# Kernel optimization log

Measured on AMD Instinct MI355X. Metric: run time of the kernel, lower is better.

The kernel has to match this reference:

```python
import jax, jax.numpy as jnp
import numpy as np

DMODEL = 1024
Q_HEADS = 16
KV_HEADS = 4
DHEAD = 64
SEQ = 2048
TOP_K = 64
ROPE_BASE = 10000.0
NEG_INF = -1e30  # stand-in for -inf that is safe under softmax


def rope_cos_sin(seq_len, dhead, base):
    inv_freq = 1.0 / (base ** (jnp.arange(0, dhead, 2, dtype=jnp.float32) / dhead))  # [dhead/2]
    t = jnp.arange(seq_len, dtype=jnp.float32)
    angles = jnp.outer(t, inv_freq)                       # [S, dhead/2]
    emb = jnp.concatenate([angles, angles], axis=-1)      # [S, dhead]
    return jnp.cos(emb), jnp.sin(emb)


def rotate_half(x):
    x1, x2 = jnp.split(x, 2, axis=-1)
    return jnp.concatenate([-x2, x1], axis=-1)


def apply_rope(x, cos, sin):
    # x: [B, H, S, dhead]; cos/sin: [S, dhead]
    return x * cos[None, None] + rotate_half(x) * sin[None, None]


def setup_inputs() -> dict:
    key = jax.random.key(0)
    ks = jax.random.split(key, 5)
    s = 0.02
    return {
        "x": jax.random.normal(ks[0], (1, SEQ, DMODEL), jnp.float32),
        "Wq": jax.random.normal(ks[1], (Q_HEADS * DHEAD, DMODEL), jnp.float32) * s,
        "Wk": jax.random.normal(ks[2], (KV_HEADS * DHEAD, DMODEL), jnp.float32) * s,
        "Wv": jax.random.normal(ks[3], (KV_HEADS * DHEAD, DMODEL), jnp.float32) * s,
        "Wo": jax.random.normal(ks[4], (DMODEL, Q_HEADS * DHEAD), jnp.float32) * s,
    }


def reference(x, Wq, Wk, Wv, Wo):
    B, S, _ = x.shape
    cos, sin = rope_cos_sin(S, DHEAD, ROPE_BASE)

    q = (x @ Wq.T).reshape(B, S, Q_HEADS, DHEAD).transpose(0, 2, 1, 3)   # [B,Hq,S,d]
    k = (x @ Wk.T).reshape(B, S, KV_HEADS, DHEAD).transpose(0, 2, 1, 3)  # [B,Hkv,S,d]
    v = (x @ Wv.T).reshape(B, S, KV_HEADS, DHEAD).transpose(0, 2, 1, 3)

    q = apply_rope(q, cos, sin)
    k = apply_rope(k, cos, sin)

    groups = Q_HEADS // KV_HEADS  # repeat_kv
    k = jnp.repeat(k, groups, axis=1)  # [B,Hq,S,d]
    v = jnp.repeat(v, groups, axis=1)

    scores = jnp.einsum("bhqd,bhkd->bhqk", q, k) / np.sqrt(DHEAD)  # [B,H,S,S]

    causal_mask = jnp.triu(jnp.ones((S, S), bool), k=1)
    scores = jnp.where(causal_mask[None, None], NEG_INF, scores)

    # top-k mask before softmax
    topk_vals, _ = jax.lax.top_k(scores, TOP_K)            # [B,H,S,K]
    threshold = topk_vals[..., -1:]                         # kth largest
    scores = jnp.where(scores < threshold, NEG_INF, scores)

    weights = jax.nn.softmax(scores, axis=-1)
    out = jnp.einsum("bhqk,bhkd->bhqd", weights, v)         # [B,H,S,d]
    out = out.transpose(0, 2, 1, 3).reshape(B, S, Q_HEADS * DHEAD)
    return out @ Wo.T
```

## Files before the change

### kernel.cpp

```cpp
#include <hip/hip_runtime.h>
#include <hip/hip_bf16.h>
#include <math.h>

#define SEQ 2048
#define DMODEL 1024
#define QH 16
#define KVH 4
#define DH 64
#define TOPK 64
#define KV_D (KVH * DH)
#define CAP 128
#define SROW 1028

typedef __attribute__((ext_vector_type(8))) short short8;
typedef __attribute__((ext_vector_type(4))) float floatx4;

__device__ __forceinline__ unsigned f2u(float f) {
    unsigned u = __float_as_uint(f);
    return (u & 0x80000000u) ? ~u : (u | 0x80000000u);
}
__device__ __forceinline__ float u2f(unsigned u) {
    unsigned v = (u & 0x80000000u) ? (u & 0x7fffffffu) : ~u;
    return __uint_as_float(v);
}
__device__ __forceinline__ unsigned short f2bf(float x) {
    unsigned u = __float_as_uint(x);
    return (unsigned short)((u + 0x7fffu + ((u >> 16) & 1u)) >> 16);
}
__device__ __forceinline__ float bf2f(unsigned short h) {
    return __uint_as_float((unsigned)h << 16);
}
__device__ __forceinline__ void split4(float4 f, ushort4& h, ushort4& l) {
    h.x = f2bf(f.x); l.x = f2bf(f.x - bf2f(h.x));
    h.y = f2bf(f.y); l.y = f2bf(f.y - bf2f(h.y));
    h.z = f2bf(f.z); l.z = f2bf(f.z - bf2f(h.z));
    h.w = f2bf(f.w); l.w = f2bf(f.w - bf2f(h.w));
}

__global__ __launch_bounds__(256) void cvt_all(const float* __restrict__ x,
                                               const float* __restrict__ Wq,
                                               const float* __restrict__ Wk,
                                               const float* __restrict__ Wv,
                                               const float* __restrict__ Wo,
                                               unsigned short* __restrict__ xhi,
                                               unsigned short* __restrict__ xlo,
                                               unsigned short* __restrict__ wbhi,
                                               unsigned short* __restrict__ wblo,
                                               unsigned short* __restrict__ wo) {
    int idx = blockIdx.x * 256 + threadIdx.x;
    if (idx >= 1179648) return;
    float4 f;
    ushort4 h, l;
    if (idx < 524288) {
        f = ((const float4*)x)[idx];
        split4(f, h, l);
        ((ushort4*)xhi)[idx] = h;
        ((ushort4*)xlo)[idx] = l;
    } else if (idx < 786432) {
        int s = idx - 524288;
        f = ((const float4*)Wq)[s];
        split4(f, h, l);
        ((ushort4*)wbhi)[s] = h;
        ((ushort4*)wblo)[s] = l;
    } else if (idx < 851968) {
        int s = idx - 786432;
        f = ((const float4*)Wk)[s];
        split4(f, h, l);
        ((ushort4*)wbhi)[idx - 524288] = h;
        ((ushort4*)wblo)[idx - 524288] = l;
    } else if (idx < 917504) {
        int s = idx - 851968;
        f = ((const float4*)Wv)[s];
        split4(f, h, l);
        ((ushort4*)wbhi)[idx - 524288] = h;
        ((ushort4*)wblo)[idx - 524288] = l;
    } else {
        int s = idx - 917504;
        f = ((const float4*)Wo)[s];
        ushort4 o;
        o.x = f2bf(f.x); o.y = f2bf(f.y); o.z = f2bf(f.z); o.w = f2bf(f.w);
        ((ushort4*)wo)[s] = o;
    }
}

__global__ __launch_bounds__(256) void sincos_lut(float* __restrict__ cosT,
                                                  float* __restrict__ sinT) {
    int idx = blockIdx.x * 256 + threadIdx.x;
    if (idx >= SEQ * 32) return;
    int t = idx >> 5, d = idx & 31;
    float inv = powf(10000.0f, -(float)d * (1.0f / 32.0f));
    float s, c;
    sincosf((float)t * inv, &s, &c);
    cosT[idx] = c;
    sinT[idx] = s;
}

__device__ __forceinline__ void async16(const void* g, void* l) {
    __builtin_amdgcn_global_load_lds(
        (const __attribute__((address_space(1))) unsigned int*)g,
        (__attribute__((address_space(3))) unsigned int*)l, 16, 0, 0);
}

__global__ __launch_bounds__(256, 2) void gemm_qkv(const unsigned short* __restrict__ Ah,
                                                   const unsigned short* __restrict__ Al,
                                                   const unsigned short* __restrict__ Bh,
                                                   const unsigned short* __restrict__ Bl,
                                                   const float* __restrict__ cosT,
                                                   const float* __restrict__ sinT,
                                                   unsigned short* __restrict__ qhi,
                                                   unsigned short* __restrict__ qlo,
                                                   unsigned short* __restrict__ khi,
                                                   unsigned short* __restrict__ klo,
                                                   float* __restrict__ vv) {
    const int K = DMODEL;
    __shared__ unsigned short lAh[128 * 32];
    __shared__ unsigned short lAl[128 * 32];
    __shared__ unsigned short lBh[128 * 32];
    __shared__ unsigned short lBl[128 * 32];
    const int tid = threadIdx.x;
    const int lane = tid & 63;
    const int wid = tid >> 6;
    const int m0 = blockIdx.y * 128, n0 = blockIdx.x * 128;
    const int mq = (wid >> 1) * 64, nq = (wid & 1) * 64;

    floatx4 acc[4][4];
#pragma unroll
    for (int a = 0; a < 4; ++a)
#pragma unroll
        for (int b = 0; b < 4; ++b) acc[a][b] = (floatx4){0.f, 0.f, 0.f, 0.f};

    const int srow = tid >> 2;
    const int skb = (tid & 3) ^ ((tid >> 3) & 3);
    const size_t goff = (size_t)srow * K + skb * 8;
    const size_t goff2 = goff + (size_t)64 * K;
    const unsigned short* pAh = Ah + (size_t)m0 * K;
    const unsigned short* pAl = Al + (size_t)m0 * K;
    const unsigned short* pBh = Bh + (size_t)n0 * K;
    const unsigned short* pBl = Bl + (size_t)n0 * K;
    unsigned lbase = __builtin_amdgcn_readfirstlane((unsigned)(wid * 1024));

    for (int k0 = 0; k0 < K; k0 += 32) {
        async16(pAh + goff + k0, (char*)lAh + lbase);
        async16(pAh + goff2 + k0, (char*)lAh + lbase + 4096);
        async16(pAl + goff + k0, (char*)lAl + lbase);
        async16(pAl + goff2 + k0, (char*)lAl + lbase + 4096);
        async16(pBh + goff + k0, (char*)lBh + lbase);
        async16(pBh + goff2 + k0, (char*)lBh + lbase + 4096);
        async16(pBl + goff + k0, (char*)lBl + lbase);
        async16(pBl + goff2 + k0, (char*)lBl + lbase + 4096);
        __syncthreads();

        short8 ah[4], al[4], bh[4], bl[4];
#pragma unroll
        for (int mt = 0; mt < 4; ++mt) {
            int row = mq + mt * 16 + (lane & 15);
            int s = ((lane >> 4) ^ ((row >> 1) & 3)) * 8;
            ah[mt] = *(const short8*)&lAh[row * 32 + s];
            al[mt] = *(const short8*)&lAl[row * 32 + s];
        }
#pragma unroll
        for (int nt = 0; nt < 4; ++nt) {
            int row = nq + nt * 16 + (lane & 15);
            int s = ((lane >> 4) ^ ((row >> 1) & 3)) * 8;
            bh[nt] = *(const short8*)&lBh[row * 32 + s];
            bl[nt] = *(const short8*)&lBl[row * 32 + s];
        }
#pragma unroll
        for (int mt = 0; mt < 4; ++mt)
#pragma unroll
            for (int nt = 0; nt < 4; ++nt) {
                floatx4 a = acc[mt][nt];
                a = __builtin_amdgcn_mfma_f32_16x16x32_bf16(al[mt], bh[nt], a, 0, 0, 0);
                a = __builtin_amdgcn_mfma_f32_16x16x32_bf16(ah[mt], bl[nt], a, 0, 0, 0);
                a = __builtin_amdgcn_mfma_f32_16x16x32_bf16(ah[mt], bh[nt], a, 0, 0, 0);
                acc[mt][nt] = a;
            }
        __syncthreads();
    }

    if (n0 < 1280) {
        const bool isq = (n0 < 1024);
#pragma unroll
        for (int mt = 0; mt < 4; ++mt)
#pragma unroll
            for (int nt = 0; nt < 2; ++nt) {
                const int d32 = nt * 16 + (lane & 15);
#pragma unroll
                for (int rr = 0; rr < 4; ++rr) {
                    int row = m0 + mq + mt * 16 + (lane >> 4) * 4 + rr;
                    float lo = acc[mt][nt][rr], hi = acc[mt][nt + 2][rr];
                    float c = cosT[row * 32 + d32], s = sinT[row * 32 + d32];
                    float rlo = lo * c - hi * s;
                    float rhi = hi * c + lo * s;
                    unsigned short hlo = f2bf(rlo), hhi = f2bf(rhi);
                    unsigned short llo = f2bf(rlo - bf2f(hlo));
                    unsigned short lhi = f2bf(rhi - bf2f(hhi));
                    if (isq) {
                        size_t o = (size_t)row * DMODEL + n0 + nq + d32;
                        qhi[o] = hlo; qhi[o + 32] = hhi;
                        qlo[o] = llo; qlo[o + 32] = lhi;
                    } else {
                        int kvh = (n0 + nq - 1024) >> 6;
                        size_t o = ((size_t)kvh * SEQ + row) * DH + d32;
                        khi[o] = hlo; khi[o + 32] = hhi;
                        klo[o] = llo; klo[o + 32] = lhi;
                    }
                }
            }
    } else {
#pragma unroll
        for (int mt = 0; mt < 4; ++mt)
#pragma unroll
            for (int nt = 0; nt < 4; ++nt) {
                int vcol = n0 + nq + nt * 16 + (lane & 15) - 1280;
                int rbase = m0 + mq + mt * 16 + (lane >> 4) * 4;
#pragma unroll
                for (int rr = 0; rr < 4; ++rr)
                    vv[(size_t)(rbase + rr) * KV_D + vcol] = acc[mt][nt][rr];
            }
    }
}

__global__ __launch_bounds__(256, 2) void gemm_mfma(const unsigned short* __restrict__ A,
                                                    const unsigned short* __restrict__ B,
                                                    float* __restrict__ C,
                                                    int M, int N, int K) {
    __shared__ unsigned short ldsA[128 * 32];
    __shared__ unsigned short ldsB[128 * 32];
    const int tid = threadIdx.x;
    const int lane = tid & 63;
    const int wid = tid >> 6;
    const int m0 = blockIdx.y * 128, n0 = blockIdx.x * 128;
    const int mq = (wid >> 1) * 64, nq = (wid & 1) * 64;

    floatx4 acc[4][4];
#pragma unroll
    for (int a = 0; a < 4; ++a)
#pragma unroll
        for (int b = 0; b < 4; ++b) acc[a][b] = (floatx4){0.f, 0.f, 0.f, 0.f};

    const int srow = tid >> 2;
    const int skb = (tid & 3) ^ ((tid >> 3) & 3);
    const unsigned short* Ag = A + (size_t)(m0 + srow) * K + skb * 8;
    const unsigned short* Bg = B + (size_t)(n0 + srow) * K + skb * 8;
    unsigned lbase = __builtin_amdgcn_readfirstlane((unsigned)(wid * 1024));
    char* la = (char*)ldsA + lbase;
    char* lb = (char*)ldsB + lbase;

    for (int k0 = 0; k0 < K; k0 += 32) {
        async16(Ag + k0, la);
        async16(Ag + (size_t)64 * K + k0, la + 4096);
        async16(Bg + k0, lb);
        async16(Bg + (size_t)64 * K + k0, lb + 4096);
        __syncthreads();

        short8 af[4], bf[4];
#pragma unroll
        for (int mt = 0; mt < 4; ++mt) {
            int row = mq + mt * 16 + (lane & 15);
            int s = ((lane >> 4) ^ ((row >> 1) & 3)) * 8;
            af[mt] = *(const short8*)&ldsA[row * 32 + s];
        }
#pragma unroll
        for (int nt = 0; nt < 4; ++nt) {
            int row = nq + nt * 16 + (lane & 15);
            int s = ((lane >> 4) ^ ((row >> 1) & 3)) * 8;
            bf[nt] = *(const short8*)&ldsB[row * 32 + s];
        }
#pragma unroll
        for (int mt = 0; mt < 4; ++mt)
#pragma unroll
            for (int nt = 0; nt < 4; ++nt)
                acc[mt][nt] = __builtin_amdgcn_mfma_f32_16x16x32_bf16(af[mt], bf[nt], acc[mt][nt], 0, 0, 0);
        __syncthreads();
    }
#pragma unroll
    for (int mt = 0; mt < 4; ++mt)
#pragma unroll
        for (int nt = 0; nt < 4; ++nt) {
            int col = n0 + nq + nt * 16 + (lane & 15);
            int rbase = m0 + mq + mt * 16 + (lane >> 4) * 4;
#pragma unroll
            for (int rr = 0; rr < 4; ++rr)
                C[(size_t)(rbase + rr) * N + col] = acc[mt][nt][rr];
        }
}

__device__ __forceinline__ void av_group(float w, int jbase, const float* __restrict__ vb,
                                         float& acc) {
    unsigned long long mk = __ballot(w > 0.f);
    while (mk) {
        int l = __ffsll((unsigned long long)mk) - 1;
        mk &= mk - 1;
        float wj = __shfl(w, l, 64);
        acc += wj * vb[(size_t)(jbase + l * 4) * KV_D];
    }
}

__device__ __forceinline__ void score_chunk(const unsigned short* __restrict__ khi,
                                            const unsigned short* __restrict__ klo,
                                            float* __restrict__ S,
                                            const short8& ah0, const short8& ah1,
                                            const short8& al0, const short8& al1,
                                            int kvh, int w, int lane, int imax, int cbase) {
    const int koff = (lane >> 4) * 8;
#pragma unroll
    for (int n = 0; n < 4; ++n) {
        int jbi = cbase + w + n * 16;
        int jb = jbi * 16;
        if (jb <= imax) {
            size_t bidx = ((size_t)kvh * SEQ + jb + (lane & 15)) * DH + koff;
            short8 bh0 = *(const short8*)(khi + bidx);
            short8 bh1 = *(const short8*)(khi + bidx + 32);
            short8 bl0 = *(const short8*)(klo + bidx);
            short8 bl1 = *(const short8*)(klo + bidx + 32);
            floatx4 acc = (floatx4){0.f, 0.f, 0.f, 0.f};
            acc = __builtin_amdgcn_mfma_f32_16x16x32_bf16(al0, bh0, acc, 0, 0, 0);
            acc = __builtin_amdgcn_mfma_f32_16x16x32_bf16(al1, bh1, acc, 0, 0, 0);
            acc = __builtin_amdgcn_mfma_f32_16x16x32_bf16(ah0, bl0, acc, 0, 0, 0);
            acc = __builtin_amdgcn_mfma_f32_16x16x32_bf16(ah1, bl1, acc, 0, 0, 0);
            acc = __builtin_amdgcn_mfma_f32_16x16x32_bf16(ah0, bh0, acc, 0, 0, 0);
            acc = __builtin_amdgcn_mfma_f32_16x16x32_bf16(ah1, bh1, acc, 0, 0, 0);
            int col = (jb & 1023) + (lane & 15);
            int rbase = (lane >> 4) * 4;
#pragma unroll
            for (int rr = 0; rr < 4; ++rr)
                S[(size_t)(rbase + rr) * SROW + col] = acc[rr] * 0.125f;
        }
    }
}

__global__ __launch_bounds__(1024, 8) void attn_block(const unsigned short* __restrict__ qhi,
                                                      const unsigned short* __restrict__ qlo,
                                                      const unsigned short* __restrict__ khi,
                                                      const unsigned short* __restrict__ klo,
                                                      const float* __restrict__ v,
                                                      unsigned short* __restrict__ outb) {
    extern __shared__ float S[];
    const int lane = threadIdx.x & 63;
    const int w = threadIdx.x >> 6;
    const int t = 127 - blockIdx.x;
    const int h = blockIdx.y;
    const int kvh = h >> 2;
    const int m0 = t * 16;
    const int imax = m0 + 15;

    const int arow = m0 + (lane & 15);
    const int koff = (lane >> 4) * 8;
    size_t aidx = (size_t)arow * DMODEL + h * DH + koff;
    short8 ah0 = *(const short8*)(qhi + aidx);
    short8 ah1 = *(const short8*)(qhi + aidx + 32);
    short8 al0 = *(const short8*)(qlo + aidx);
    short8 al1 = *(const short8*)(qlo + aidx + 32);

    const int irow = m0 + w;
    const int cmax = (irow >> 8) + 1;
    float* Srow = S + (size_t)w * SROW;
    uint4 uv[8];
#pragma unroll
    for (int c = 0; c < 8; ++c) uv[c] = make_uint4(0u, 0u, 0u, 0u);

    score_chunk(khi, klo, S, ah0, ah1, al0, al1, kvh, w, lane, imax, 0);
    __syncthreads();
#pragma unroll
    for (int c = 0; c < 4; ++c) {
        if (c < cmax) {
            const int j0 = c * 256 + lane * 4;
            float4 f = *(const float4*)&Srow[j0];
            uv[c].x = (j0 + 0 <= irow) ? f2u(f.x) : 0u;
            uv[c].y = (j0 + 1 <= irow) ? f2u(f.y) : 0u;
            uv[c].z = (j0 + 2 <= irow) ? f2u(f.z) : 0u;
            uv[c].w = (j0 + 3 <= irow) ? f2u(f.w) : 0u;
        }
    }
    __syncthreads();

    if (imax >= 1024) {
        score_chunk(khi, klo, S, ah0, ah1, al0, al1, kvh, w, lane, imax, 64);
    }
    __syncthreads();
#pragma unroll
    for (int c = 4; c < 8; ++c) {
        if (c < cmax) {
            const int j0 = (c - 4) * 256 + lane * 4;
            float4 f = *(const float4*)&Srow[j0];
            int jg = c * 256 + lane * 4;
            uv[c].x = (jg + 0 <= irow) ? f2u(f.x) : 0u;
            uv[c].y = (jg + 1 <= irow) ? f2u(f.y) : 0u;
            uv[c].z = (jg + 2 <= irow) ? f2u(f.z) : 0u;
            uv[c].w = (jg + 3 <= irow) ? f2u(f.w) : 0u;
        }
    }
    __syncthreads();

    float2* pl = (float2*)S + w * CAP;

    unsigned lmax = 0u;
#pragma unroll
    for (int c = 0; c < 8; ++c)
        lmax = max(lmax, max(max(uv[c].x, uv[c].y), max(uv[c].z, uv[c].w)));
    unsigned um = lmax, Lb = lmax;
#pragma unroll
    for (int o = 32; o > 0; o >>= 1) {
        um = max(um, (unsigned)__shfl_xor((int)um, o, 64));
        Lb = min(Lb, (unsigned)__shfl_xor((int)Lb, o, 64));
    }
    const float mf = u2f(um);

    unsigned p = 1u;
    if (irow >= TOPK) {
        unsigned diff = Lb ^ um;
        if (diff == 0u) {
            p = um;
        } else {
            int hb = 31 - __builtin_clz(diff);
            p = (hb >= 31) ? 0u : ((um >> (hb + 1)) << (hb + 1));
            for (int b = hb; b >= 0; --b) {
                unsigned cand = p | (1u << b);
                int cnt = 0;
#pragma unroll
                for (int c = 0; c < 8; ++c) {
                    if (c < cmax) {
                        cnt += __popcll(__ballot(uv[c].x >= cand));
                        cnt += __popcll(__ballot(uv[c].y >= cand));
                        cnt += __popcll(__ballot(uv[c].z >= cand));
                        cnt += __popcll(__ballot(uv[c].w >= cand));
                    }
                }
                if (cnt >= TOPK) p = cand;
            }
        }
    }

    const unsigned long long lmask = (lane == 0) ? 0ull : (~0ull >> (64 - lane));
    int base = 0;
#pragma unroll
    for (int c = 0; c < 8; ++c) {
        if (c < cmax) {
#pragma unroll
            for (int e = 0; e < 4; ++e) {
                unsigned u = (e == 0) ? uv[c].x : (e == 1) ? uv[c].y : (e == 2) ? uv[c].z : uv[c].w;
                bool keep = (u >= p);
                unsigned long long mk = __ballot(keep);
                if (keep) {
                    int pos = base + __popcll(mk & lmask);
                    if (pos < CAP)
                        pl[pos] = make_float2(__expf(u2f(u) - mf),
                                              __int_as_float(c * 256 + lane * 4 + e));
                }
                base += (int)__popcll(mk);
            }
        }
    }

    const float* vb = v + kvh * DH + lane;
    float acc = 0.f, den = 0.f;
    if (base <= CAP) {
        int l = 0;
        for (; l + 16 <= base; l += 16) {
            float2 pr[16];
            float vx[16];
#pragma unroll
            for (int u = 0; u < 16; ++u) pr[u] = pl[l + u];
#pragma unroll
            for (int u = 0; u < 16; ++u)
                vx[u] = vb[(size_t)__float_as_int(pr[u].y) * KV_D];
#pragma unroll
            for (int u = 0; u < 16; ++u) { den += pr[u].x; acc += pr[u].x * vx[u]; }
        }
        for (; l < base; ++l) {
            float2 pp = pl[l];
            den += pp.x;
            acc += pp.x * vb[(size_t)__float_as_int(pp.y) * KV_D];
        }
    } else {
        float lsum = 0.f;
#pragma unroll
        for (int c = 0; c < 8; ++c) {
            if (c < cmax) {
                float w0 = (uv[c].x >= p) ? __expf(u2f(uv[c].x) - mf) : 0.f;
                float w1 = (uv[c].y >= p) ? __expf(u2f(uv[c].y) - mf) : 0.f;
                float w2 = (uv[c].z >= p) ? __expf(u2f(uv[c].z) - mf) : 0.f;
                float w3 = (uv[c].w >= p) ? __expf(u2f(uv[c].w) - mf) : 0.f;
                lsum += (w0 + w1) + (w2 + w3);
                av_group(w0, c * 256 + 0, vb, acc);
                av_group(w1, c * 256 + 1, vb, acc);
                av_group(w2, c * 256 + 2, vb, acc);
                av_group(w3, c * 256 + 3, vb, acc);
            }
        }
        den = lsum;
#pragma unroll
        for (int o = 32; o > 0; o >>= 1) den += __shfl_xor(den, o, 64);
    }

    outb[(size_t)irow * DMODEL + h * DH + lane] = f2bf(acc / den);
}

extern "C" void kernel_launch(void* const* d_in, const int* in_sizes, int n_in,
                              void* d_out, int out_size, void* d_ws, size_t ws_size,
                              hipStream_t stream) {
    const float* x  = (const float*)d_in[0];
    const float* Wq = (const float*)d_in[1];
    const float* Wk = (const float*)d_in[2];
    const float* Wv = (const float*)d_in[3];
    const float* Wo = (const float*)d_in[4];
    float* out = (float*)d_out;

    float* ws = (float*)d_ws;
    float* vv   = ws;
    float* cosT = vv + (size_t)SEQ * KV_D;
    float* sinT = cosT + SEQ * 32;
    unsigned short* bfp = (unsigned short*)(sinT + SEQ * 32);
    unsigned short* xhi  = bfp;  bfp += (size_t)SEQ * DMODEL;
    unsigned short* xlo  = bfp;  bfp += (size_t)SEQ * DMODEL;
    unsigned short* wbhi = bfp;  bfp += (size_t)1536 * DMODEL;
    unsigned short* wblo = bfp;  bfp += (size_t)1536 * DMODEL;
    unsigned short* wob  = bfp;  bfp += (size_t)DMODEL * DMODEL;
    unsigned short* qhi  = bfp;  bfp += (size_t)SEQ * DMODEL;
    unsigned short* qlo  = bfp;  bfp += (size_t)SEQ * DMODEL;
    unsigned short* khi  = bfp;  bfp += (size_t)KVH * SEQ * DH;
    unsigned short* klo  = bfp;  bfp += (size_t)KVH * SEQ * DH;
    unsigned short* attnb = xhi;

    dim3 blk(256);

    cvt_all<<<(1179648 + 255) / 256, blk, 0, stream>>>(x, Wq, Wk, Wv, Wo,
                                                       xhi, xlo, wbhi, wblo, wob);
    sincos_lut<<<(SEQ * 32 + 255) / 256, blk, 0, stream>>>(cosT, sinT);

    gemm_qkv<<<dim3(1536 / 128, SEQ / 128), blk, 0, stream>>>(xhi, xlo, wbhi, wblo,
                                                              cosT, sinT,
                                                              qhi, qlo, khi, klo, vv);

    const int attn_lds = 16 * SROW * 4;
    hipFuncSetAttribute((const void*)attn_block,
                        hipFuncAttributeMaxDynamicSharedMemorySize, attn_lds);
    attn_block<<<dim3(SEQ / 16, QH), dim3(1024), attn_lds, stream>>>(qhi, qlo, khi, klo, vv, attnb);

    gemm_mfma<<<dim3(DMODEL / 128, SEQ / 128), blk, 0, stream>>>(attnb, wob, out, SEQ, DMODEL, DMODEL);
}
```

Measured before the change: 317.4 us.

## Fuse RoPE table into conversion, skip V split-precision, compact top-k candidates, retile Wo GEMM

The sin/cos table is now built inside the conversion kernel, which removes one launch. The V projection tiles use only the high bf16 halves, which drops the split-precision loads and two of the three MFMAs for those tiles at some cost in V precision. The 1/sqrt(d) scale moves from the score store into the RoPE epilogue of Q. Attention first compacts every score at or above a per-lane lower bound into LDS (up to 512 entries) and runs the radix threshold search over that shorter list. The output GEMM uses 64x128 tiles so more blocks are launched.

```diff
diff --git a/kernel.cpp b/kernel.cpp
--- a/kernel.cpp
+++ b/kernel.cpp
@@ -9,7 +9,7 @@
 #define DH 64
 #define TOPK 64
 #define KV_D (KVH * DH)
-#define CAP 128
+#define CCAP 512
 #define SROW 1028
 
 typedef __attribute__((ext_vector_type(8))) short short8;
@@ -46,9 +46,11 @@
                                                unsigned short* __restrict__ xlo,
                                                unsigned short* __restrict__ wbhi,
                                                unsigned short* __restrict__ wblo,
-                                               unsigned short* __restrict__ wo) {
+                                               unsigned short* __restrict__ wo,
+                                               float* __restrict__ cosT,
+                                               float* __restrict__ sinT) {
     int idx = blockIdx.x * 256 + threadIdx.x;
-    if (idx >= 1179648) return;
+    if (idx >= 1196032) return;
     float4 f;
     ushort4 h, l;
     if (idx < 524288) {
@@ -74,25 +76,29 @@
         split4(f, h, l);
         ((ushort4*)wbhi)[idx - 524288] = h;
         ((ushort4*)wblo)[idx - 524288] = l;
-    } else {
+    } else if (idx < 1179648) {
         int s = idx - 917504;
         f = ((const float4*)Wo)[s];
         ushort4 o;
         o.x = f2bf(f.x); o.y = f2bf(f.y); o.z = f2bf(f.z); o.w = f2bf(f.w);
         ((ushort4*)wo)[s] = o;
-    }
-}
-
-__global__ __launch_bounds__(256) void sincos_lut(float* __restrict__ cosT,
-                                                  float* __restrict__ sinT) {
-    int idx = blockIdx.x * 256 + threadIdx.x;
-    if (idx >= SEQ * 32) return;
-    int t = idx >> 5, d = idx & 31;
-    float inv = powf(10000.0f, -(float)d * (1.0f / 32.0f));
-    float s, c;
-    sincosf((float)t * inv, &s, &c);
-    cosT[idx] = c;
-    sinT[idx] = s;
+    } else {
+        int s = idx - 1179648;
+        int e0 = s * 4;
+        float ft = (float)(e0 >> 5);
+        int d0 = e0 & 31;
+        float4 cw, sw;
+#pragma unroll
+        for (int k = 0; k < 4; ++k) {
+            float inv = powf(10000.0f, -(float)(d0 + k) * (1.0f / 32.0f));
+            float ss, cc;
+            sincosf(ft * inv, &ss, &cc);
+            ((float*)&cw)[k] = cc;
+            ((float*)&sw)[k] = ss;
+        }
+        ((float4*)cosT)[s] = cw;
+        ((float4*)sinT)[s] = sw;
+    }
 }
 
 __device__ __forceinline__ void async16(const void* g, void* l) {
@@ -122,6 +128,7 @@
     const int wid = tid >> 6;
     const int m0 = blockIdx.y * 128, n0 = blockIdx.x * 128;
     const int mq = (wid >> 1) * 64, nq = (wid & 1) * 64;
+    const bool isv = (n0 >= 1280);
 
     floatx4 acc[4][4];
 #pragma unroll
@@ -142,12 +149,14 @@
     for (int k0 = 0; k0 < K; k0 += 32) {
         async16(pAh + goff + k0, (char*)lAh + lbase);
         async16(pAh + goff2 + k0, (char*)lAh + lbase + 4096);
-        async16(pAl + goff + k0, (char*)lAl + lbase);
-        async16(pAl + goff2 + k0, (char*)lAl + lbase + 4096);
         async16(pBh + goff + k0, (char*)lBh + lbase);
         async16(pBh + goff2 + k0, (char*)lBh + lbase + 4096);
-        async16(pBl + goff + k0, (char*)lBl + lbase);
-        async16(pBl + goff2 + k0, (char*)lBl + lbase + 4096);
+        if (!isv) {
+            async16(pAl + goff + k0, (char*)lAl + lbase);
+            async16(pAl + goff2 + k0, (char*)lAl + lbase + 4096);
+            async16(pBl + goff + k0, (char*)lBl + lbase);
+            async16(pBl + goff2 + k0, (char*)lBl + lbase + 4096);
+        }
         __syncthreads();
 
         short8 ah[4], al[4], bh[4], bl[4];
@@ -156,30 +165,39 @@
             int row = mq + mt * 16 + (lane & 15);
             int s = ((lane >> 4) ^ ((row >> 1) & 3)) * 8;
             ah[mt] = *(const short8*)&lAh[row * 32 + s];
-            al[mt] = *(const short8*)&lAl[row * 32 + s];
+            if (!isv) al[mt] = *(const short8*)&lAl[row * 32 + s];
         }
 #pragma unroll
         for (int nt = 0; nt < 4; ++nt) {
             int row = nq + nt * 16 + (lane & 15);
             int s = ((lane >> 4) ^ ((row >> 1) & 3)) * 8;
             bh[nt] = *(const short8*)&lBh[row * 32 + s];
-            bl[nt] = *(const short8*)&lBl[row * 32 + s];
-        }
-#pragma unroll
-        for (int mt = 0; mt < 4; ++mt)
-#pragma unroll
-            for (int nt = 0; nt < 4; ++nt) {
-                floatx4 a = acc[mt][nt];
-                a = __builtin_amdgcn_mfma_f32_16x16x32_bf16(al[mt], bh[nt], a, 0, 0, 0);
-                a = __builtin_amdgcn_mfma_f32_16x16x32_bf16(ah[mt], bl[nt], a, 0, 0, 0);
-                a = __builtin_amdgcn_mfma_f32_16x16x32_bf16(ah[mt], bh[nt], a, 0, 0, 0);
-                acc[mt][nt] = a;
-            }
+            if (!isv) bl[nt] = *(const short8*)&lBl[row * 32 + s];
+        }
+        if (isv) {
+#pragma unroll
+            for (int mt = 0; mt < 4; ++mt)
+#pragma unroll
+                for (int nt = 0; nt < 4; ++nt)
+                    acc[mt][nt] = __builtin_amdgcn_mfma_f32_16x16x32_bf16(ah[mt], bh[nt], acc[mt][nt], 0, 0, 0);
+        } else {
+#pragma unroll
+            for (int mt = 0; mt < 4; ++mt)
+#pragma unroll
+                for (int nt = 0; nt < 4; ++nt) {
+                    floatx4 a = acc[mt][nt];
+                    a = __builtin_amdgcn_mfma_f32_16x16x32_bf16(al[mt], bh[nt], a, 0, 0, 0);
+                    a = __builtin_amdgcn_mfma_f32_16x16x32_bf16(ah[mt], bl[nt], a, 0, 0, 0);
+                    a = __builtin_amdgcn_mfma_f32_16x16x32_bf16(ah[mt], bh[nt], a, 0, 0, 0);
+                    acc[mt][nt] = a;
+                }
+        }
         __syncthreads();
     }
 
-    if (n0 < 1280) {
+    if (!isv) {
         const bool isq = (n0 < 1024);
+        const float qsc = isq ? 0.125f : 1.0f;
 #pragma unroll
         for (int mt = 0; mt < 4; ++mt)
 #pragma unroll
@@ -190,8 +208,8 @@
                     int row = m0 + mq + mt * 16 + (lane >> 4) * 4 + rr;
                     float lo = acc[mt][nt][rr], hi = acc[mt][nt + 2][rr];
                     float c = cosT[row * 32 + d32], s = sinT[row * 32 + d32];
-                    float rlo = lo * c - hi * s;
-                    float rhi = hi * c + lo * s;
+                    float rlo = (lo * c - hi * s) * qsc;
+                    float rhi = (hi * c + lo * s) * qsc;
                     unsigned short hlo = f2bf(rlo), hhi = f2bf(rhi);
                     unsigned short llo = f2bf(rlo - bf2f(hlo));
                     unsigned short lhi = f2bf(rhi - bf2f(hhi));
@@ -221,65 +239,61 @@
     }
 }
 
-__global__ __launch_bounds__(256, 2) void gemm_mfma(const unsigned short* __restrict__ A,
-                                                    const unsigned short* __restrict__ B,
-                                                    float* __restrict__ C,
-                                                    int M, int N, int K) {
-    __shared__ unsigned short ldsA[128 * 32];
-    __shared__ unsigned short ldsB[128 * 32];
+__global__ __launch_bounds__(256, 2) void gemm_wo(const unsigned short* __restrict__ A,
+                                                  const unsigned short* __restrict__ B,
+                                                  float* __restrict__ C) {
+    const int N = DMODEL, K = DMODEL;
+    __shared__ unsigned short lAs[64 * 32];
+    __shared__ unsigned short lBs[128 * 32];
     const int tid = threadIdx.x;
     const int lane = tid & 63;
     const int wid = tid >> 6;
-    const int m0 = blockIdx.y * 128, n0 = blockIdx.x * 128;
-    const int mq = (wid >> 1) * 64, nq = (wid & 1) * 64;
-
-    floatx4 acc[4][4];
+    const int m0 = blockIdx.y * 64, n0 = blockIdx.x * 128;
+
+    floatx4 acc[4][2];
 #pragma unroll
     for (int a = 0; a < 4; ++a)
 #pragma unroll
-        for (int b = 0; b < 4; ++b) acc[a][b] = (floatx4){0.f, 0.f, 0.f, 0.f};
+        for (int b = 0; b < 2; ++b) acc[a][b] = (floatx4){0.f, 0.f, 0.f, 0.f};
 
     const int srow = tid >> 2;
     const int skb = (tid & 3) ^ ((tid >> 3) & 3);
     const unsigned short* Ag = A + (size_t)(m0 + srow) * K + skb * 8;
     const unsigned short* Bg = B + (size_t)(n0 + srow) * K + skb * 8;
     unsigned lbase = __builtin_amdgcn_readfirstlane((unsigned)(wid * 1024));
-    char* la = (char*)ldsA + lbase;
-    char* lb = (char*)ldsB + lbase;
 
     for (int k0 = 0; k0 < K; k0 += 32) {
-        async16(Ag + k0, la);
-        async16(Ag + (size_t)64 * K + k0, la + 4096);
-        async16(Bg + k0, lb);
-        async16(Bg + (size_t)64 * K + k0, lb + 4096);
+        async16(Ag + k0, (char*)lAs + lbase);
+        async16(Bg + k0, (char*)lBs + lbase);
+        async16(Bg + (size_t)64 * K + k0, (char*)lBs + lbase + 4096);
         __syncthreads();
 
-        short8 af[4], bf[4];
+        short8 af[4], bf[2];
 #pragma unroll
         for (int mt = 0; mt < 4; ++mt) {
-            int row = mq + mt * 16 + (lane & 15);
+            int row = mt * 16 + (lane & 15);
             int s = ((lane >> 4) ^ ((row >> 1) & 3)) * 8;
-            af[mt] = *(const short8*)&ldsA[row * 32 + s];
-        }
-#pragma unroll
-        for (int nt = 0; nt < 4; ++nt) {
-            int row = nq + nt * 16 + (lane & 15);
+            af[mt] = *(const short8*)&lAs[row * 32 + s];
+        }
+#pragma unroll
+        for (int nt = 0; nt < 2; ++nt) {
+            int row = wid * 32 + nt * 16 + (lane & 15);
             int s = ((lane >> 4) ^ ((row >> 1) & 3)) * 8;
-            bf[nt] = *(const short8*)&ldsB[row * 32 + s];
+            bf[nt] = *(const short8*)&lBs[row * 32 + s];
         }
 #pragma unroll
         for (int mt = 0; mt < 4; ++mt)
 #pragma unroll
-            for (int nt = 0; nt < 4; ++nt)
+            for (int nt = 0; nt < 2; ++nt)
                 acc[mt][nt] = __builtin_amdgcn_mfma_f32_16x16x32_bf16(af[mt], bf[nt], acc[mt][nt], 0, 0, 0);
         __syncthreads();
     }
 #pragma unroll
     for (int mt = 0; mt < 4; ++mt)
 #pragma unroll
-        for (int nt = 0; nt < 4; ++nt) {
-            int col = n0 + nq + nt * 16 + (lane & 15);
-            int rbase = m0 + mq + mt * 16 + (lane >> 4) * 4;
+        for (int nt = 0; nt < 2; ++nt) {
+            int col = n0 + wid * 32 + nt * 16 + (lane & 15);
+            int rbase = m0 + mt * 16 + (lane >> 4) * 4;
 #pragma unroll
             for (int rr = 0; rr < 4; ++rr)
                 C[(size_t)(rbase + rr) * N + col] = acc[mt][nt][rr];
@@ -325,7 +339,7 @@
             int rbase = (lane >> 4) * 4;
 #pragma unroll
             for (int rr = 0; rr < 4; ++rr)
-                S[(size_t)(rbase + rr) * SROW + col] = acc[rr] * 0.125f;
+                S[(size_t)(rbase + rr) * SROW + col] = acc[rr];
         }
     }
 }
@@ -393,8 +407,6 @@
     }
     __syncthreads();
 
-    float2* pl = (float2*)S + w * CAP;
-
     unsigned lmax = 0u;
 #pragma unroll
     for (int c = 0; c < 8; ++c)
@@ -406,58 +418,78 @@
         Lb = min(Lb, (unsigned)__shfl_xor((int)Lb, o, 64));
     }
     const float mf = u2f(um);
-
-    unsigned p = 1u;
-    if (irow >= TOPK) {
-        unsigned diff = Lb ^ um;
-        if (diff == 0u) {
-            p = um;
-        } else {
-            int hb = 31 - __builtin_clz(diff);
-            p = (hb >= 31) ? 0u : ((um >> (hb + 1)) << (hb + 1));
-            for (int b = hb; b >= 0; --b) {
-                unsigned cand = p | (1u << b);
-                int cnt = 0;
-#pragma unroll
-                for (int c = 0; c < 8; ++c) {
-                    if (c < cmax) {
-                        cnt += __popcll(__ballot(uv[c].x >= cand));
-                        cnt += __popcll(__ballot(uv[c].y >= cand));
-                        cnt += __popcll(__ballot(uv[c].z >= cand));
-                        cnt += __popcll(__ballot(uv[c].w >= cand));
-                    }
-                }
-                if (cnt >= TOPK) p = cand;
-            }
-        }
-    }
-
     const unsigned long long lmask = (lane == 0) ? 0ull : (~0ull >> (64 - lane));
-    int base = 0;
+
+    uint2* cand = (uint2*)Srow;
+    const unsigned thr0 = Lb ? Lb : 1u;
+    int nc = 0;
 #pragma unroll
     for (int c = 0; c < 8; ++c) {
         if (c < cmax) {
 #pragma unroll
             for (int e = 0; e < 4; ++e) {
                 unsigned u = (e == 0) ? uv[c].x : (e == 1) ? uv[c].y : (e == 2) ? uv[c].z : uv[c].w;
-                bool keep = (u >= p);
-                unsigned long long mk = __ballot(keep);
-                if (keep) {
-                    int pos = base + __popcll(mk & lmask);
-                    if (pos < CAP)
-                        pl[pos] = make_float2(__expf(u2f(u) - mf),
-                                              __int_as_float(c * 256 + lane * 4 + e));
+                bool kp = (u >= thr0);
+                unsigned long long mk = __ballot(kp);
+                if (kp) {
+                    int pos = nc + __popcll(mk & lmask);
+                    if (pos < CCAP)
+                        cand[pos] = make_uint2(u, (unsigned)(c * 256 + lane * 4 + e));
                 }
-                base += (int)__popcll(mk);
+                nc += (int)__popcll(mk);
             }
         }
     }
 
     const float* vb = v + kvh * DH + lane;
     float acc = 0.f, den = 0.f;
-    if (base <= CAP) {
+
+    if (nc <= CCAP) {
+        unsigned cu[8];
+#pragma unroll
+        for (int tt = 0; tt < 8; ++tt) {
+            int idx = tt * 64 + lane;
+            unsigned uu = cand[idx].x;
+            cu[tt] = (idx < nc) ? uu : 0u;
+        }
+
+        unsigned p = 1u;
+        if (irow >= TOPK) {
+            unsigned diff = Lb ^ um;
+            if (diff == 0u) {
+                p = um;
+            } else {
+                int hb = 31 - __builtin_clz(diff);
+                p = (hb >= 31) ? 0u : ((um >> (hb + 1)) << (hb + 1));
+                for (int b = hb; b >= 0; --b) {
+                    unsigned cv = p | (1u << b);
+                    int cnt = 0;
+#pragma unroll
+                    for (int tt = 0; tt < 8; ++tt)
+                        cnt += __popcll(__ballot(cu[tt] >= cv));
+                    if (cnt >= TOPK) p = cv;
+                }
+            }
+        }
+
+        int kc = 0;
+#pragma unroll
+        for (int tt = 0; tt < 8; ++tt) {
+            int idx = tt * 64 + lane;
+            uint2 e = cand[idx];
+            bool kp = (idx < nc) && (e.x >= p);
+            unsigned long long mk = __ballot(kp);
+            if (kp) {
+                int pos = kc + __popcll(mk & lmask);
+                ((float2*)cand)[pos] = make_float2(__expf(u2f(e.x) - mf),
+                                                   __uint_as_float(e.y));
+            }
+            kc += (int)__popcll(mk);
+        }
+
+        float2* pl = (float2*)cand;
         int l = 0;
-        for (; l + 16 <= base; l += 16) {
+        for (; l + 16 <= kc; l += 16) {
             float2 pr[16];
             float vx[16];
 #pragma unroll
@@ -468,30 +500,84 @@
 #pragma unroll
             for (int u = 0; u < 16; ++u) { den += pr[u].x; acc += pr[u].x * vx[u]; }
         }
-        for (; l < base; ++l) {
+        for (; l < kc; ++l) {
             float2 pp = pl[l];
             den += pp.x;
             acc += pp.x * vb[(size_t)__float_as_int(pp.y) * KV_D];
         }
     } else {
-        float lsum = 0.f;
+        unsigned p = 1u;
+        if (irow >= TOPK) {
+            unsigned diff = Lb ^ um;
+            if (diff == 0u) {
+                p = um;
+            } else {
+                int hb = 31 - __builtin_clz(diff);
+                p = (hb >= 31) ? 0u : ((um >> (hb + 1)) << (hb + 1));
+                for (int b = hb; b >= 0; --b) {
+                    unsigned cv = p | (1u << b);
+                    int cnt = 0;
+#pragma unroll
+                    for (int c = 0; c < 8; ++c) {
+                        if (c < cmax) {
+                            cnt += __popcll(__ballot(uv[c].x >= cv));
+                            cnt += __popcll(__ballot(uv[c].y >= cv));
+                            cnt += __popcll(__ballot(uv[c].z >= cv));
+                            cnt += __popcll(__ballot(uv[c].w >= cv));
+                        }
+                    }
+                    if (cnt >= TOPK) p = cv;
+                }
+            }
+        }
+
+        float2* pl = (float2*)Srow;
+        int base = 0;
 #pragma unroll
         for (int c = 0; c < 8; ++c) {
             if (c < cmax) {
-                float w0 = (uv[c].x >= p) ? __expf(u2f(uv[c].x) - mf) : 0.f;
-                float w1 = (uv[c].y >= p) ? __expf(u2f(uv[c].y) - mf) : 0.f;
-                float w2 = (uv[c].z >= p) ? __expf(u2f(uv[c].z) - mf) : 0.f;
-                float w3 = (uv[c].w >= p) ? __expf(u2f(uv[c].w) - mf) : 0.f;
-                lsum += (w0 + w1) + (w2 + w3);
-                av_group(w0, c * 256 + 0, vb, acc);
-                av_group(w1, c * 256 + 1, vb, acc);
-                av_group(w2, c * 256 + 2, vb, acc);
-                av_group(w3, c * 256 + 3, vb, acc);
-            }
-        }
-        den = lsum;
-#pragma unroll
-        for (int o = 32; o > 0; o >>= 1) den += __shfl_xor(den, o, 64);
+#pragma unroll
+                for (int e = 0; e < 4; ++e) {
+                    unsigned u = (e == 0) ? uv[c].x : (e == 1) ? uv[c].y : (e == 2) ? uv[c].z : uv[c].w;
+                    bool kp = (u >= p);
+                    unsigned long long mk = __ballot(kp);
+                    if (kp) {
+                        int pos = base + __popcll(mk & lmask);
+                        if (pos < CCAP)
+                            pl[pos] = make_float2(__expf(u2f(u) - mf),
+                                                  __int_as_float(c * 256 + lane * 4 + e));
+                    }
+                    base += (int)__popcll(mk);
+                }
+            }
+        }
+
+        if (base <= CCAP) {
+            for (int l = 0; l < base; ++l) {
+                float2 pp = pl[l];
+                den += pp.x;
+                acc += pp.x * vb[(size_t)__float_as_int(pp.y) * KV_D];
+            }
+        } else {
+            float lsum = 0.f;
+#pragma unroll
+            for (int c = 0; c < 8; ++c) {
+                if (c < cmax) {
+                    float w0 = (uv[c].x >= p) ? __expf(u2f(uv[c].x) - mf) : 0.f;
+                    float w1 = (uv[c].y >= p) ? __expf(u2f(uv[c].y) - mf) : 0.f;
+                    float w2 = (uv[c].z >= p) ? __expf(u2f(uv[c].z) - mf) : 0.f;
+                    float w3 = (uv[c].w >= p) ? __expf(u2f(uv[c].w) - mf) : 0.f;
+                    lsum += (w0 + w1) + (w2 + w3);
+                    av_group(w0, c * 256 + 0, vb, acc);
+                    av_group(w1, c * 256 + 1, vb, acc);
+                    av_group(w2, c * 256 + 2, vb, acc);
+                    av_group(w3, c * 256 + 3, vb, acc);
+                }
+            }
+            den = lsum;
+#pragma unroll
+            for (int o = 32; o > 0; o >>= 1) den += __shfl_xor(den, o, 64);
+        }
     }
 
     outb[(size_t)irow * DMODEL + h * DH + lane] = f2bf(acc / den);
@@ -525,9 +611,9 @@
 
     dim3 blk(256);
 
-    cvt_all<<<(1179648 + 255) / 256, blk, 0, stream>>>(x, Wq, Wk, Wv, Wo,
-                                                       xhi, xlo, wbhi, wblo, wob);
-    sincos_lut<<<(SEQ * 32 + 255) / 256, blk, 0, stream>>>(cosT, sinT);
+    cvt_all<<<(1196032 + 255) / 256, blk, 0, stream>>>(x, Wq, Wk, Wv, Wo,
+                                                       xhi, xlo, wbhi, wblo, wob,
+                                                       cosT, sinT);
 
     gemm_qkv<<<dim3(1536 / 128, SEQ / 128), blk, 0, stream>>>(xhi, xlo, wbhi, wblo,
                                                               cosT, sinT,
@@ -538,5 +624,5 @@
                         hipFuncAttributeMaxDynamicSharedMemorySize, attn_lds);
     attn_block<<<dim3(SEQ / 16, QH), dim3(1024), attn_lds, stream>>>(qhi, qlo, khi, klo, vv, attnb);
 
-    gemm_mfma<<<dim3(DMODEL / 128, SEQ / 128), blk, 0, stream>>>(attnb, wob, out, SEQ, DMODEL, DMODEL);
-}
+    gemm_wo<<<dim3(DMODEL / 128, SEQ / 64), blk, 0, stream>>>(attnb, wob, out);
+}
```

Result: no change. 318.4 us (+0.3%).
